# Kernel optimization log

Measured on AMD Instinct MI355X. Metric: run time of the kernel, lower is better.

The kernel has to match this reference:

```python
import jax, jax.numpy as jnp
import numpy as np

N = 20000   # nodes
E = 320000  # edges
H = 256     # hidden size == input size (no FeatEncoder branch)


def setup_inputs() -> dict:
    key = jax.random.key(0)
    ks = jax.random.split(key, 10)
    x = jax.random.normal(ks[0], (N, H), dtype=jnp.float32)
    edge_index = jax.random.randint(ks[1], (2, E), 0, N, dtype=jnp.int32)
    s = 1.0 / np.sqrt(H)  # PyG Linear default (glorot-ish uniform)
    inp = {"x": x, "edge_index": edge_index}
    for i, name in enumerate(["W1", "W1_1", "W2", "W3"]):
        inp[name] = jax.random.uniform(ks[2 + i], (H, H), jnp.float32, -s, s)
    for name in ["b1", "b1_1", "b2", "b3"]:
        inp[name] = jnp.zeros((H,), jnp.float32)
    return inp


def gcn_norm(edge_index, num_nodes):
    # add self loops (weight 1.0), symmetric normalization D^-1/2 A D^-1/2
    row, col = edge_index[0], edge_index[1]
    loop = jnp.arange(num_nodes, dtype=row.dtype)
    row = jnp.concatenate([row, loop])
    col = jnp.concatenate([col, loop])
    w = jnp.ones(row.shape[0], dtype=jnp.float32)
    deg = jax.ops.segment_sum(w, col, num_segments=num_nodes)  # in-degree at targets
    dinv = jnp.where(deg > 0, jax.lax.rsqrt(deg), 0.0)
    norm = dinv[row] * dinv[col]  # [E+N]
    return row, col, norm


def conv(x, W, b, row, col, norm, num_nodes):
    # GCNConv: linear transform, gather-scale-scatter-add, bias
    h = x @ W                                   # [N, H]
    msg = norm[:, None] * h[row]                # [E+N, H] gather + scale
    out = jax.ops.segment_sum(msg, col, num_segments=num_nodes)  # scatter-add
    return out + b


def reference(x, edge_index, W1, b1, W1_1, b1_1, W2, b2, W3, b3):
    num_nodes = x.shape[0]
    row, col, norm = gcn_norm(edge_index, num_nodes)
    h1 = jax.nn.relu(conv(x, W1, b1, row, col, norm, num_nodes))
    h2 = jax.nn.relu(conv(h1, W1_1, b1_1, row, col, norm, num_nodes))
    out2 = conv(h2, W2, b2, row, col, norm, num_nodes)
    out3 = conv(h2, W3, b3, row, col, norm, num_nodes)
    return out2, out3
```

## Files before the change

### kernel.cpp

```cpp
#include <hip/hip_runtime.h>
#include <math.h>

#define HD 256

typedef short bf16x8 __attribute__((ext_vector_type(8)));
typedef float f32x4  __attribute__((ext_vector_type(4)));

__device__ __forceinline__ unsigned short f2bf(float f) {
    unsigned u = __builtin_bit_cast(unsigned, f);
    unsigned r = (u + 0x7fffu + ((u >> 16) & 1u)) >> 16;
    return (unsigned short)r;
}
__device__ __forceinline__ float bf2f(unsigned b) {
    return __builtin_bit_cast(float, (b & 0xffffu) << 16);
}



__global__ void fill_edges_kernel(const int* __restrict__ ei, int E,
                                  int* __restrict__ cursor, int* __restrict__ csr) {
    int idx = blockIdx.x * blockDim.x + threadIdx.x;
    if (idx >= E) return;
    int r = ei[idx];
    int c = ei[E + idx];
    int slot = atomicAdd(&cursor[c], 1);
    if (slot < 127) csr[(c << 7) + slot] = r;
}

__global__ void finalize_kernel(int* __restrict__ cursor, int* __restrict__ csr,
                                float* __restrict__ dinv, int n) {
    int v = blockIdx.x * blockDim.x + threadIdx.x;
    if (v >= n) return;
    int c = min(cursor[v], 126);
    csr[(v << 7) + c] = v;
    cursor[v] = c + 1;
    dinv[v] = rsqrtf((float)(c + 1));
}


__global__ __launch_bounds__(256) void prep_kernel(const float* __restrict__ W0,
                                                   const float* __restrict__ W1,
                                                   const float* __restrict__ W2,
                                                   const float* __restrict__ W3,
                                                   unsigned short* __restrict__ pkhi,
                                                   unsigned short* __restrict__ pklo,
                                                   const float* __restrict__ x,
                                                   const float* __restrict__ dinv,
                                                   unsigned short* __restrict__ T, int N) {
    const int bid = blockIdx.x;
    if (bid < 128) {
        int gid = bid * 256 + threadIdx.x;
        int mat  = gid >> 13;
        int rem  = gid & 8191;
        int nc   = rem >> 9;
        int kc   = (rem >> 6) & 7;
        int lane = rem & 63;
        const float* W = (mat == 0) ? W0 : (mat == 1) ? W1 : (mat == 2) ? W2 : W3;
        int col = nc * 16 + (lane & 15);
        int kb  = kc * 32 + (lane >> 4) * 8;
        alignas(16) unsigned short h[8], l[8];
#pragma unroll
        for (int e = 0; e < 8; ++e) {
            float w = W[(size_t)(kb + e) * HD + col];
            unsigned short hb = f2bf(w);
            h[e] = hb;
            l[e] = f2bf(w - bf2f(hb));
        }
        size_t off = (size_t)mat * 65536 + ((size_t)(nc * 8 + kc) * 64 + lane) * 8;
        *(uint4*)&pkhi[off] = *(const uint4*)h;
        *(uint4*)&pklo[off] = *(const uint4*)l;
    } else {
        int gid = (bid - 128) * 256 + threadIdx.x;
        if (gid >= N * 32) return;
        int row = gid >> 5;
        int q   = gid & 31;
        float s = dinv[row];
        const float4* xp = (const float4*)(x + (size_t)row * HD + q * 8);
        float4 v0 = xp[0], v1 = xp[1];
        float vals[8] = {v0.x, v0.y, v0.z, v0.w, v1.x, v1.y, v1.z, v1.w};
        alignas(16) unsigned short h[8], l[8];
#pragma unroll
        for (int e = 0; e < 8; ++e) {
            float t = vals[e] * s;
            unsigned short hb = f2bf(t);
            h[e] = hb;
            l[e] = f2bf(t - bf2f(hb));
        }
        size_t o = (size_t)row * 512 + (size_t)(q >> 2) * 64 + (q & 3) * 8;
        *(uint4*)&T[o]      = *(const uint4*)h;
        *(uint4*)&T[o + 32] = *(const uint4*)l;
    }
}


template<int OUTMODE>
__global__ __launch_bounds__(256) void agg_chunk_kernel(const float* __restrict__ zin,
                                                        const int* __restrict__ csr,
                                                        const int* __restrict__ cnt,
                                                        const float* __restrict__ dinv,
                                                        const float* __restrict__ bias,
                                                        void* __restrict__ outBuf, int N) {
    const int chunk = blockIdx.x & 7;
    const int nb    = blockIdx.x >> 3;
    const int wave  = threadIdx.x >> 6;
    const int lane  = threadIdx.x & 63;
    const int slot  = lane & 7;
    const int ni    = lane >> 3;

    int v = nb * 32 + wave * 8 + ni;
    const bool valid = v < N;
    if (!valid) v = N - 1;

    const int beg = v << 7;
    const int end = beg + cnt[v];
    const float dv = dinv[v];

    const float4* zp = (const float4*)zin;
    const size_t cbase = (size_t)chunk * 8 + slot;

    float a0 = 0.f, a1 = 0.f, a2 = 0.f, a3 = 0.f;
    int i = beg;
    for (; i + 4 <= end; i += 4) {
        int u0 = csr[i], u1 = csr[i + 1], u2 = csr[i + 2], u3 = csr[i + 3];
        float4 d0 = zp[(size_t)u0 * 64 + cbase];
        float4 d1 = zp[(size_t)u1 * 64 + cbase];
        float4 d2 = zp[(size_t)u2 * 64 + cbase];
        float4 d3 = zp[(size_t)u3 * 64 + cbase];
        a0 += (d0.x + d1.x) + (d2.x + d3.x);
        a1 += (d0.y + d1.y) + (d2.y + d3.y);
        a2 += (d0.z + d1.z) + (d2.z + d3.z);
        a3 += (d0.w + d1.w) + (d2.w + d3.w);
    }
    for (; i < end; ++i) {
        int u = csr[i];
        float4 d = zp[(size_t)u * 64 + cbase];
        a0 += d.x; a1 += d.y; a2 += d.z; a3 += d.w;
    }
    if (!valid) return;

    float t0, t1, t2, t3;
    if (OUTMODE == 2) {
        t0 = dv * a0; t1 = dv * a1; t2 = dv * a2; t3 = dv * a3;
    } else {
        float4 bv = *(const float4*)&bias[chunk * 32 + slot * 4];
        t0 = dv * fmaxf(fmaf(dv, a0, bv.x), 0.f);
        t1 = dv * fmaxf(fmaf(dv, a1, bv.y), 0.f);
        t2 = dv * fmaxf(fmaf(dv, a2, bv.z), 0.f);
        t3 = dv * fmaxf(fmaf(dv, a3, bv.w), 0.f);
    }

    if (OUTMODE == 1) {
        ((float4*)outBuf)[(size_t)v * 64 + cbase] = make_float4(t0, t1, t2, t3);
    } else {
        unsigned short h0 = f2bf(t0), h1 = f2bf(t1), h2 = f2bf(t2), h3 = f2bf(t3);
        uint2 hw, lw;
        hw.x = h0 | ((unsigned)h1 << 16);
        hw.y = h2 | ((unsigned)h3 << 16);
        unsigned short l0 = f2bf(t0 - bf2f(h0)), l1 = f2bf(t1 - bf2f(h1));
        unsigned short l2 = f2bf(t2 - bf2f(h2)), l3 = f2bf(t3 - bf2f(h3));
        lw.x = l0 | ((unsigned)l1 << 16);
        lw.y = l2 | ((unsigned)l3 << 16);
        unsigned short* T = (unsigned short*)outBuf;
        size_t o = (size_t)v * 512 + chunk * 64 + slot * 4;
        *(uint2*)&T[o]      = hw;
        *(uint2*)&T[o + 32] = lw;
    }
}


template<int NBY>
__global__ __launch_bounds__(256, 3)
void gemm_mfma_kernel(const unsigned short* __restrict__ T,
                      const unsigned short* __restrict__ pkhi,
                      const unsigned short* __restrict__ pklo,
                      const float* __restrict__ ba,
                      const float* __restrict__ bb,
                      float* __restrict__ Ca,
                      float* __restrict__ Cb, int M, int gx) {
    __shared__ unsigned short ldsW[2][2][2048];

    const int id  = blockIdx.x;
    const int xcd = id & 7;
    const int t   = id >> 3;
    const int by  = t & (NBY - 1);
    const int g   = t / NBY;
    const int bx  = xcd + (g << 3);
    if (bx >= gx) return;

    const int tid  = threadIdx.x;
    const int lane = tid & 63;
    const int wave = tid >> 6;

    const int sel = (NBY == 8) ? (by >> 2) : 0;
    const int nc0 = ((NBY == 8) ? (by & 3) : by) * 4;
    const unsigned short* ph = pkhi + (size_t)sel * 65536;
    const unsigned short* pl = pklo + (size_t)sel * 65536;
    float*       C    = sel ? Cb : Ca;
    const float* bias = sel ? bb : ba;

    const int row0  = bx * 128 + wave * 32;
    const int rowA0 = min(row0 + (lane & 15), M - 1);
    const int rowA1 = min(row0 + 16 + (lane & 15), M - 1);
    const int kg    = lane >> 4;

    const unsigned short* aT0 = T + (size_t)rowA0 * 512 + kg * 8;
    const unsigned short* aT1 = T + (size_t)rowA1 * 512 + kg * 8;

    const int snf = tid >> 6;
    const unsigned short* sph = ph + ((size_t)(nc0 + snf) * 8) * 512 + (size_t)(tid & 63) * 8;
    const unsigned short* spl = pl + ((size_t)(nc0 + snf) * 8) * 512 + (size_t)(tid & 63) * 8;

    f32x4 acc[2][4];
#pragma unroll
    for (int f = 0; f < 2; ++f)
#pragma unroll
        for (int j = 0; j < 4; ++j) acc[f][j] = (f32x4)0.f;

    uint4 sh = *(const uint4*)(sph);
    uint4 sl = *(const uint4*)(spl);
    *(uint4*)&ldsW[0][0][tid * 8] = sh;
    *(uint4*)&ldsW[0][1][tid * 8] = sl;
    sh = *(const uint4*)(sph + 512);
    sl = *(const uint4*)(spl + 512);

    bf16x8 a0h[2], a0l[2], a1h[2], a1l[2];
    a0h[0] = *(const bf16x8*)(aT0);
    a0l[0] = *(const bf16x8*)(aT0 + 32);
    a1h[0] = *(const bf16x8*)(aT1);
    a1l[0] = *(const bf16x8*)(aT1 + 32);
    __syncthreads();

#pragma unroll
    for (int kc = 0; kc < 8; ++kc) {
        const int cur = kc & 1;
        if (kc < 7) {
            a0h[cur ^ 1] = *(const bf16x8*)(aT0 + (kc + 1) * 64);
            a0l[cur ^ 1] = *(const bf16x8*)(aT0 + (kc + 1) * 64 + 32);
            a1h[cur ^ 1] = *(const bf16x8*)(aT1 + (kc + 1) * 64);
            a1l[cur ^ 1] = *(const bf16x8*)(aT1 + (kc + 1) * 64 + 32);
        }
        bf16x8 wh[4], wl[4];
#pragma unroll
        for (int j = 0; j < 4; ++j) {
            wh[j] = *(const bf16x8*)&ldsW[cur][0][((size_t)j * 64 + lane) * 8];
            wl[j] = *(const bf16x8*)&ldsW[cur][1][((size_t)j * 64 + lane) * 8];
        }
#pragma unroll
        for (int j = 0; j < 4; ++j) {
            acc[0][j] = __builtin_amdgcn_mfma_f32_16x16x32_bf16(a0h[cur], wh[j], acc[0][j], 0, 0, 0);
            acc[0][j] = __builtin_amdgcn_mfma_f32_16x16x32_bf16(a0h[cur], wl[j], acc[0][j], 0, 0, 0);
            acc[0][j] = __builtin_amdgcn_mfma_f32_16x16x32_bf16(a0l[cur], wh[j], acc[0][j], 0, 0, 0);
            acc[1][j] = __builtin_amdgcn_mfma_f32_16x16x32_bf16(a1h[cur], wh[j], acc[1][j], 0, 0, 0);
            acc[1][j] = __builtin_amdgcn_mfma_f32_16x16x32_bf16(a1h[cur], wl[j], acc[1][j], 0, 0, 0);
            acc[1][j] = __builtin_amdgcn_mfma_f32_16x16x32_bf16(a1l[cur], wh[j], acc[1][j], 0, 0, 0);
        }
        if (kc < 7) {
            *(uint4*)&ldsW[cur ^ 1][0][tid * 8] = sh;
            *(uint4*)&ldsW[cur ^ 1][1][tid * 8] = sl;
            if (kc < 6) {
                sh = *(const uint4*)(sph + (size_t)(kc + 2) * 512);
                sl = *(const uint4*)(spl + (size_t)(kc + 2) * 512);
            }
            __syncthreads();
        }
    }

#pragma unroll
    for (int nf = 0; nf < 4; ++nf) {
        int col = (nc0 + nf) * 16 + (lane & 15);
        float badd = (NBY == 8) ? bias[col] : 0.f;
#pragma unroll
        for (int f = 0; f < 2; ++f) {
#pragma unroll
            for (int r = 0; r < 4; ++r) {
                int row = row0 + f * 16 + kg * 4 + r;
                if (row < M) C[(size_t)row * HD + col] = acc[f][nf][r] + badd;
            }
        }
    }
}


static inline size_t align_up(size_t x, size_t a) { return (x + a - 1) & ~(a - 1); }

extern "C" void kernel_launch(void* const* d_in, const int* in_sizes, int n_in,
                              void* d_out, int out_size, void* d_ws, size_t ws_size,
                              hipStream_t stream) {
    const int N = in_sizes[0] / HD;
    const int E = in_sizes[1] / 2;

    const float* x   = (const float*)d_in[0];
    const int*   ei  = (const int*)d_in[1];
    const float* W1  = (const float*)d_in[2];
    const float* W11 = (const float*)d_in[3];
    const float* W2  = (const float*)d_in[4];
    const float* W3  = (const float*)d_in[5];
    const float* b1  = (const float*)d_in[6];
    const float* b11 = (const float*)d_in[7];
    const float* b2  = (const float*)d_in[8];
    const float* b3  = (const float*)d_in[9];

    float* out2 = (float*)d_out;
    float* out3 = out2 + (size_t)N * HD;

    char* p = (char*)d_ws;
    int*   cursor = (int*)p;   p += align_up((size_t)N * 4, 256);
    float* dinv   = (float*)p; p += align_up((size_t)N * 4, 256);
    int*   csr    = (int*)p;   p += align_up((size_t)N * 128 * 4, 256);
    unsigned short* pkhi = (unsigned short*)p; p += align_up((size_t)4 * 65536 * 2, 256);
    unsigned short* pklo = (unsigned short*)p; p += align_up((size_t)4 * 65536 * 2, 256);
    float* bufZ = (float*)p;   p += align_up((size_t)N * HD * 4, 256);
    unsigned short* bufT = (unsigned short*)p; p += align_up((size_t)N * 512 * 2, 256);
    (void)ws_size; (void)n_in; (void)out_size;

    hipMemsetAsync(cursor, 0, (size_t)N * 4, stream);
    fill_edges_kernel<<<(E + 255) / 256, 256, 0, stream>>>(ei, E, cursor, csr);
    finalize_kernel<<<(N + 255) / 256, 256, 0, stream>>>(cursor, csr, dinv, N);

    prep_kernel<<<128 + (N * 32 + 255) / 256, 256, 0, stream>>>(
        W1, W11, W2, W3, pkhi, pklo, x, dinv, bufT, N);

    const int gx  = (N + 127) / 128;
    const int gxp = ((gx + 7) / 8) * 8;
    const int aggBlocks = 8 * ((N + 31) / 32);

    gemm_mfma_kernel<4><<<gxp * 4, 256, 0, stream>>>(
        bufT, pkhi + 0 * 65536, pklo + 0 * 65536, nullptr, nullptr, bufZ, nullptr, N, gx);
    agg_chunk_kernel<0><<<aggBlocks, 256, 0, stream>>>(bufZ, csr, cursor, dinv, b1, bufT, N);

    gemm_mfma_kernel<4><<<gxp * 4, 256, 0, stream>>>(
        bufT, pkhi + 1 * 65536, pklo + 1 * 65536, nullptr, nullptr, bufZ, nullptr, N, gx);
    agg_chunk_kernel<1><<<aggBlocks, 256, 0, stream>>>(bufZ, csr, cursor, dinv, b11, bufT, N);

    agg_chunk_kernel<2><<<aggBlocks, 256, 0, stream>>>((const float*)bufT, csr, cursor, dinv,
                                                       nullptr, bufZ, N);

    gemm_mfma_kernel<8><<<gxp * 8, 256, 0, stream>>>(
        (const unsigned short*)bufZ, pkhi + 2 * 65536, pklo + 2 * 65536, b2, b3, out2, out3, N, gx);
}
```

Baseline: 196.1 us.

## Fuse setup kernels and pad CSR rows to unroll gathers by eight

Merges edge filling with weight packing, and CSR finalisation with input conversion, into two combined launches. The separate dinv buffer is dropped in favour of recomputing rsqrt from the degree count. Each CSR row is padded to a multiple of eight with a sentinel index that points at a zeroed pad row, so the aggregation loop can run eight independent gathers per iteration with no remainder loop. This trades extra loads from the zero row and slightly larger buffers for fewer launches and more memory-level parallelism in the gather.

```diff
diff --git a/kernel.cpp b/kernel.cpp
--- a/kernel.cpp
+++ b/kernel.cpp
@@ -17,39 +17,26 @@
 
 
 
-__global__ void fill_edges_kernel(const int* __restrict__ ei, int E,
-                                  int* __restrict__ cursor, int* __restrict__ csr) {
-    int idx = blockIdx.x * blockDim.x + threadIdx.x;
-    if (idx >= E) return;
-    int r = ei[idx];
-    int c = ei[E + idx];
-    int slot = atomicAdd(&cursor[c], 1);
-    if (slot < 127) csr[(c << 7) + slot] = r;
-}
-
-__global__ void finalize_kernel(int* __restrict__ cursor, int* __restrict__ csr,
-                                float* __restrict__ dinv, int n) {
-    int v = blockIdx.x * blockDim.x + threadIdx.x;
-    if (v >= n) return;
-    int c = min(cursor[v], 126);
-    csr[(v << 7) + c] = v;
-    cursor[v] = c + 1;
-    dinv[v] = rsqrtf((float)(c + 1));
-}
-
-
-__global__ __launch_bounds__(256) void prep_kernel(const float* __restrict__ W0,
-                                                   const float* __restrict__ W1,
-                                                   const float* __restrict__ W2,
-                                                   const float* __restrict__ W3,
-                                                   unsigned short* __restrict__ pkhi,
-                                                   unsigned short* __restrict__ pklo,
-                                                   const float* __restrict__ x,
-                                                   const float* __restrict__ dinv,
-                                                   unsigned short* __restrict__ T, int N) {
+__global__ __launch_bounds__(256) void fillpack_kernel(const int* __restrict__ ei, int E,
+                                                       int* __restrict__ cursor,
+                                                       int* __restrict__ csr,
+                                                       const float* __restrict__ W0,
+                                                       const float* __restrict__ W1,
+                                                       const float* __restrict__ W2,
+                                                       const float* __restrict__ W3,
+                                                       unsigned short* __restrict__ pkhi,
+                                                       unsigned short* __restrict__ pklo) {
+    const int Eb = (E + 255) >> 8;
     const int bid = blockIdx.x;
-    if (bid < 128) {
-        int gid = bid * 256 + threadIdx.x;
+    if (bid < Eb) {
+        int idx = bid * 256 + threadIdx.x;
+        if (idx >= E) return;
+        int r = ei[idx];
+        int c = ei[E + idx];
+        int slot = atomicAdd(&cursor[c], 1);
+        if (slot < 127) csr[((size_t)c << 7) + slot] = r;
+    } else {
+        int gid = (bid - Eb) * 256 + threadIdx.x;
         int mat  = gid >> 13;
         int rem  = gid & 8191;
         int nc   = rem >> 9;
@@ -69,12 +56,34 @@
         size_t off = (size_t)mat * 65536 + ((size_t)(nc * 8 + kc) * 64 + lane) * 8;
         *(uint4*)&pkhi[off] = *(const uint4*)h;
         *(uint4*)&pklo[off] = *(const uint4*)l;
-    } else {
-        int gid = (bid - 128) * 256 + threadIdx.x;
+    }
+}
+
+
+__global__ __launch_bounds__(256) void finconv_kernel(const int* __restrict__ cursor,
+                                                      int* __restrict__ csr,
+                                                      const float* __restrict__ x,
+                                                      unsigned short* __restrict__ T,
+                                                      float* __restrict__ zpad,
+                                                      float* __restrict__ tpad,
+                                                      int N) {
+    const int Fb = (N + 255) >> 8;
+    const int Cb = (N * 32 + 255) >> 8;
+    const int bid = blockIdx.x;
+    if (bid < Fb) {
+        int v = bid * 256 + threadIdx.x;
+        if (v >= N) return;
+        int c = min(cursor[v], 126);
+        size_t base = (size_t)v << 7;
+        csr[base + c] = v;
+        int pad = (c + 8) & ~7;
+        for (int s = c + 1; s < pad; ++s) csr[base + s] = N;
+    } else if (bid < Fb + Cb) {
+        int gid = (bid - Fb) * 256 + threadIdx.x;
         if (gid >= N * 32) return;
         int row = gid >> 5;
         int q   = gid & 31;
-        float s = dinv[row];
+        float s = rsqrtf((float)(min(cursor[row], 126) + 1));
         const float4* xp = (const float4*)(x + (size_t)row * HD + q * 8);
         float4 v0 = xp[0], v1 = xp[1];
         float vals[8] = {v0.x, v0.y, v0.z, v0.w, v1.x, v1.y, v1.z, v1.w};
@@ -89,6 +98,10 @@
         size_t o = (size_t)row * 512 + (size_t)(q >> 2) * 64 + (q & 3) * 8;
         *(uint4*)&T[o]      = *(const uint4*)h;
         *(uint4*)&T[o + 32] = *(const uint4*)l;
+    } else {
+        int t = threadIdx.x;
+        zpad[t] = 0.f;
+        tpad[t] = 0.f;
     }
 }
 
@@ -96,8 +109,7 @@
 template<int OUTMODE>
 __global__ __launch_bounds__(256) void agg_chunk_kernel(const float* __restrict__ zin,
                                                         const int* __restrict__ csr,
-                                                        const int* __restrict__ cnt,
-                                                        const float* __restrict__ dinv,
+                                                        const int* __restrict__ cursor,
                                                         const float* __restrict__ bias,
                                                         void* __restrict__ outBuf, int N) {
     const int chunk = blockIdx.x & 7;
@@ -111,30 +123,31 @@
     const bool valid = v < N;
     if (!valid) v = N - 1;
 
-    const int beg = v << 7;
-    const int end = beg + cnt[v];
-    const float dv = dinv[v];
+    const int cnt  = min(cursor[v], 126) + 1;
+    const float dv = rsqrtf((float)cnt);
+    const int iters = (cnt + 7) >> 3;
+    const int* cp = csr + ((size_t)v << 7);
 
     const float4* zp = (const float4*)zin;
     const size_t cbase = (size_t)chunk * 8 + slot;
 
     float a0 = 0.f, a1 = 0.f, a2 = 0.f, a3 = 0.f;
-    int i = beg;
-    for (; i + 4 <= end; i += 4) {
-        int u0 = csr[i], u1 = csr[i + 1], u2 = csr[i + 2], u3 = csr[i + 3];
+    for (int it = 0; it < iters; ++it) {
+        const int* q = cp + it * 8;
+        int u0 = q[0], u1 = q[1], u2 = q[2], u3 = q[3];
+        int u4 = q[4], u5 = q[5], u6 = q[6], u7 = q[7];
         float4 d0 = zp[(size_t)u0 * 64 + cbase];
         float4 d1 = zp[(size_t)u1 * 64 + cbase];
         float4 d2 = zp[(size_t)u2 * 64 + cbase];
         float4 d3 = zp[(size_t)u3 * 64 + cbase];
-        a0 += (d0.x + d1.x) + (d2.x + d3.x);
-        a1 += (d0.y + d1.y) + (d2.y + d3.y);
-        a2 += (d0.z + d1.z) + (d2.z + d3.z);
-        a3 += (d0.w + d1.w) + (d2.w + d3.w);
-    }
-    for (; i < end; ++i) {
-        int u = csr[i];
-        float4 d = zp[(size_t)u * 64 + cbase];
-        a0 += d.x; a1 += d.y; a2 += d.z; a3 += d.w;
+        float4 d4 = zp[(size_t)u4 * 64 + cbase];
+        float4 d5 = zp[(size_t)u5 * 64 + cbase];
+        float4 d6 = zp[(size_t)u6 * 64 + cbase];
+        float4 d7 = zp[(size_t)u7 * 64 + cbase];
+        a0 += ((d0.x + d1.x) + (d2.x + d3.x)) + ((d4.x + d5.x) + (d6.x + d7.x));
+        a1 += ((d0.y + d1.y) + (d2.y + d3.y)) + ((d4.y + d5.y) + (d6.y + d7.y));
+        a2 += ((d0.z + d1.z) + (d2.z + d3.z)) + ((d4.z + d5.z) + (d6.z + d7.z));
+        a3 += ((d0.w + d1.w) + (d2.w + d3.w)) + ((d4.w + d5.w) + (d6.w + d7.w));
     }
     if (!valid) return;
 
@@ -305,20 +318,22 @@
 
     char* p = (char*)d_ws;
     int*   cursor = (int*)p;   p += align_up((size_t)N * 4, 256);
-    float* dinv   = (float*)p; p += align_up((size_t)N * 4, 256);
     int*   csr    = (int*)p;   p += align_up((size_t)N * 128 * 4, 256);
     unsigned short* pkhi = (unsigned short*)p; p += align_up((size_t)4 * 65536 * 2, 256);
     unsigned short* pklo = (unsigned short*)p; p += align_up((size_t)4 * 65536 * 2, 256);
-    float* bufZ = (float*)p;   p += align_up((size_t)N * HD * 4, 256);
-    unsigned short* bufT = (unsigned short*)p; p += align_up((size_t)N * 512 * 2, 256);
+    float* bufZ = (float*)p;   p += align_up((size_t)(N + 1) * HD * 4, 256);
+    unsigned short* bufT = (unsigned short*)p; p += align_up((size_t)(N + 1) * 512 * 2, 256);
     (void)ws_size; (void)n_in; (void)out_size;
 
+    const int Eb = (E + 255) / 256;
+    const int Fb = (N + 255) / 256;
+    const int Cb = (N * 32 + 255) / 256;
+
     hipMemsetAsync(cursor, 0, (size_t)N * 4, stream);
-    fill_edges_kernel<<<(E + 255) / 256, 256, 0, stream>>>(ei, E, cursor, csr);
-    finalize_kernel<<<(N + 255) / 256, 256, 0, stream>>>(cursor, csr, dinv, N);
-
-    prep_kernel<<<128 + (N * 32 + 255) / 256, 256, 0, stream>>>(
-        W1, W11, W2, W3, pkhi, pklo, x, dinv, bufT, N);
+    fillpack_kernel<<<Eb + 128, 256, 0, stream>>>(ei, E, cursor, csr, W1, W11, W2, W3, pkhi, pklo);
+    finconv_kernel<<<Fb + Cb + 1, 256, 0, stream>>>(cursor, csr, x, bufT,
+                                                    bufZ + (size_t)N * HD,
+                                                    (float*)(bufT + (size_t)N * 512), N);
 
     const int gx  = (N + 127) / 128;
     const int gxp = ((gx + 7) / 8) * 8;
@@ -326,13 +341,13 @@
 
     gemm_mfma_kernel<4><<<gxp * 4, 256, 0, stream>>>(
         bufT, pkhi + 0 * 65536, pklo + 0 * 65536, nullptr, nullptr, bufZ, nullptr, N, gx);
-    agg_chunk_kernel<0><<<aggBlocks, 256, 0, stream>>>(bufZ, csr, cursor, dinv, b1, bufT, N);
+    agg_chunk_kernel<0><<<aggBlocks, 256, 0, stream>>>(bufZ, csr, cursor, b1, bufT, N);
 
     gemm_mfma_kernel<4><<<gxp * 4, 256, 0, stream>>>(
         bufT, pkhi + 1 * 65536, pklo + 1 * 65536, nullptr, nullptr, bufZ, nullptr, N, gx);
-    agg_chunk_kernel<1><<<aggBlocks, 256, 0, stream>>>(bufZ, csr, cursor, dinv, b11, bufT, N);
-
-    agg_chunk_kernel<2><<<aggBlocks, 256, 0, stream>>>((const float*)bufT, csr, cursor, dinv,
+    agg_chunk_kernel<1><<<aggBlocks, 256, 0, stream>>>(bufZ, csr, cursor, b11, bufT, N);
+
+    agg_chunk_kernel<2><<<aggBlocks, 256, 0, stream>>>((const float*)bufT, csr, cursor,
                                                        nullptr, bufZ, N);
 
     gemm_mfma_kernel<8><<<gxp * 8, 256, 0, stream>>>(
```

New measurement: 187.9 us. -4.2%, faster.
